# Performance work log

Measured on AMD Instinct MI355X. Metric: run time of the kernel, lower is better.

Reference implementation:

```python
import jax, jax.numpy as jnp
import numpy as np


def _gcn(x, ei, W, b):
    """PyG-style GCNConv: add self-loops, symmetric deg^-1/2 normalization,
    linear transform, scatter-sum aggregation at target nodes, then bias."""
    n = x.shape[0]
    loops = jnp.arange(n)
    src = jnp.concatenate([ei[0], loops])  # message sources
    dst = jnp.concatenate([ei[1], loops])  # aggregation targets
    deg = jax.ops.segment_sum(jnp.ones(src.shape[0], x.dtype), dst, num_segments=n)
    dinv = jnp.where(deg > 0, jax.lax.rsqrt(deg), jnp.zeros_like(deg))
    h = x @ W  # [N, H]
    norm = (dinv[src] * dinv[dst])[:, None]
    out = jax.ops.segment_sum(h[src] * norm, dst, num_segments=n)
    return out + b


def setup_inputs() -> dict:
    N, E, C, H, O, HOPS = 50000, 1600000, 256, 256, 40, 3
    key = jax.random.key(0)
    ks = jax.random.split(key, 12)

    def xav(k, shp):
        # xavier_uniform with relu gain, as in init_weights
        fan_in, fan_out = shp[-2], shp[-1]
        lim = float(np.sqrt(2.0) * np.sqrt(6.0 / (fan_in + fan_out)))
        return jax.random.uniform(k, shp, jnp.float32, -lim, lim)

    return {
        "x": jax.random.normal(ks[0], (N, C), jnp.float32),
        "edge_index": jax.random.randint(ks[1], (2, E), 0, N),
        "new_edge_indexs": jax.random.randint(ks[2], (HOPS, 2, E), 0, N),
        "W_mlp": xav(ks[3], (C, H)),
        "b_mlp": jnp.zeros((H,), jnp.float32),
        "We1": xav(ks[4], (C, H)),
        "be1": jnp.zeros((H,), jnp.float32),
        "We2": xav(ks[5], (H, H)),
        "be2": jnp.zeros((H,), jnp.float32),
        "Wh": xav(ks[6], (HOPS, C, H)),
        "bh": jnp.zeros((HOPS, H), jnp.float32),
        "att": jnp.ones((HOPS + 2,), jnp.float32),
        "Wc": xav(ks[7], (H * (HOPS + 2), O)),
        "bc": jnp.zeros((O,), jnp.float32),
    }


def reference(x, edge_index, new_edge_indexs, W_mlp, b_mlp, We1, be1, We2, be2,
              Wh, bh, att, Wc, bc):
    hops = Wh.shape[0]
    mask = jax.nn.softmax(att)  # softmax over branch attention weights

    mlp = jax.nn.relu(x @ W_mlp + b_mlp) * mask[0]

    e = jax.nn.relu(_gcn(x, edge_index, We1, be1))
    # dropout(p=0.5) is identity in eval mode
    e = jax.nn.relu(_gcn(e, edge_index, We2, be2)) * mask[1]

    # NOTE: original code uses mask[i+1] per hop (hop 0 shares mask[1] with extra_conv)
    outs = [jax.nn.relu(_gcn(x, new_edge_indexs[i], Wh[i], bh[i])) * mask[i + 1]
            for i in range(hops)]

    z = jnp.concatenate(outs + [e, mlp], axis=1)  # [N, H*(hops+2)]
    z = z @ Wc + bc
    return jax.nn.log_softmax(z, axis=-1)
```

## Files before the change

kernel.cpp:

```cpp
#include <hip/hip_runtime.h>
#include <hip/hip_bf16.h>

typedef unsigned short u16;
typedef unsigned int u32;
typedef unsigned char u8;

typedef __bf16 bf16x8 __attribute__((ext_vector_type(8)));
typedef float f32x4 __attribute__((ext_vector_type(4)));

__device__ __forceinline__ u16 f2b(float f) {
    u32 u = __float_as_uint(f);
    u32 r = u + 0x7fffu + ((u >> 16) & 1u);
    return (u16)(r >> 16);
}
__device__ __forceinline__ u8 f2e4m3(float v) {
    return (u8)(__builtin_amdgcn_cvt_pk_fp8_f32(v, v, 0, false) & 0xff);
}
__device__ __forceinline__ void acc16(float* a, uint4 v) {
    u32 w[4] = {v.x, v.y, v.z, v.w};
#pragma unroll
    for (int q = 0; q < 4; ++q) {
        auto p0 = __builtin_amdgcn_cvt_pk_f32_fp8(w[q], false);
        auto p1 = __builtin_amdgcn_cvt_pk_f32_fp8(w[q], true);
        a[q * 4 + 0] += p0[0]; a[q * 4 + 1] += p0[1];
        a[q * 4 + 2] += p1[0]; a[q * 4 + 3] += p1[1];
    }
}

#define SA 72
#define BSHIFT 8
#define BMAX 256
#define BCAP 12288
#define BINCHUNK 4096
#define GEMM_SMEM (128 * SA * 2 * 2)

__global__ __launch_bounds__(256) void prep(
    const int* __restrict__ ei, const int* __restrict__ nei, int E, int B, int SETS,
    int* __restrict__ bcnt, u32* __restrict__ binned, int binB,
    const float* __restrict__ x, u16* __restrict__ x16, int PB, int N,
    const float* __restrict__ W_mlp, const float* __restrict__ We1,
    const float* __restrict__ We2, const float* __restrict__ Wh,
    u16* __restrict__ wt, int HOPS,
    const float* __restrict__ Wc, u16* __restrict__ wct, int O, int NB, int WCB,
    const float* __restrict__ att, float* __restrict__ mask) {
    __shared__ u32 ebuf[BINCHUNK];
    __shared__ int hist[BMAX], resv[BMAX], lbase[BMAX], lcur[BMAX], s[BMAX];
    int b = blockIdx.x, t = threadIdx.x;
    if (b < binB * SETS) {
        int cx = b / SETS, set = b % SETS;
        const int* src = (set == 0) ? ei : (nei + (size_t)(set - 1) * 2 * E);
        const int* dst = src + E;
        hist[t] = 0; lcur[t] = 0;
        __syncthreads();
        int base = cx * BINCHUNK;
        int lim = min(base + BINCHUNK, E);
        for (int i = base + t; i < lim; i += 256)
            atomicAdd(&hist[dst[i] >> BSHIFT], 1);
        __syncthreads();
        int h = hist[t];
        if (t < B && h > 0) resv[t] = atomicAdd(&bcnt[set * BMAX + t], h);
        s[t] = h;
        __syncthreads();
        for (int off = 1; off < 256; off <<= 1) {
            int x2 = s[t];
            int add = (t >= off) ? s[t - off] : 0;
            __syncthreads();
            s[t] = x2 + add;
            __syncthreads();
        }
        lbase[t] = s[t] - h;
        __syncthreads();
        for (int i = base + t; i < lim; i += 256) {
            int d = dst[i];
            int bb = d >> BSHIFT;
            int p = atomicAdd(&lcur[bb], 1);
            ebuf[lbase[bb] + p] = (u32)src[i] | ((u32)d << 16);
        }
        __syncthreads();
        int cnt = lim - base;
        for (int i = t; i < cnt; i += 256) {
            u32 pk = ebuf[i];
            int bb = (int)(pk >> (16 + BSHIFT));
            int gpos = resv[bb] + (i - lbase[bb]);
            if (gpos < BCAP)
                binned[((size_t)set * BMAX + bb) * BCAP + gpos] = pk;
        }
        return;
    }
    b -= binB * SETS;
    if (b < PB) {
        long g = (long)b * 256 + t;
        if (g * 4 < (long)N * 256) {
            float4 v = reinterpret_cast<const float4*>(x)[g];
            ushort4 o; o.x = f2b(v.x); o.y = f2b(v.y); o.z = f2b(v.z); o.w = f2b(v.w);
            reinterpret_cast<ushort4*>(x16)[g] = o;
        }
        return;
    }
    b -= PB;
    int WB = (3 + HOPS) * 256;
    if (b < WB) {
        int y = b >> 8, ib = b & 255;
        const float* W = (y == 0) ? W_mlp : (y == 1) ? We1 : (y == 2) ? We2
                                          : (Wh + (size_t)(y - 3) * 65536);
        int idx = ib * 256 + t;
        int n = idx >> 8, k = idx & 255;
        wt[(size_t)y * 65536 + idx] = f2b(W[k * 256 + n]);
        return;
    }
    b -= WB;
    if (b < WCB) {
        int idx = b * 256 + t;
        if (idx < NB * 48 * 256) {
            int bb = idx / (48 * 256), r = idx - bb * 48 * 256;
            int n = r >> 8, k = r & 255;
            float v = (n < O) ? Wc[((size_t)(bb * 256 + k)) * O + n] : 0.f;
            wct[idx] = f2b(v);
        }
        return;
    }
    if (t == 0) {
        float m = -3.4e38f;
        for (int i = 0; i < NB; ++i) m = fmaxf(m, att[i]);
        float s2 = 0.f;
        for (int i = 0; i < NB; ++i) { float e = __expf(att[i] - m); mask[i] = e; s2 += e; }
        for (int i = 0; i < NB; ++i) mask[i] /= s2;
    }
}

__global__ void bscan(const int* __restrict__ bcnt, int* __restrict__ bbase,
                      int* __restrict__ rp, int N, int E, int B) {
    int set = blockIdx.x, t = threadIdx.x;
    int v = (t < B) ? bcnt[set * BMAX + t] : 0;
    __shared__ int s[256];
    s[t] = v; __syncthreads();
    for (int off = 1; off < 256; off <<= 1) {
        int x = s[t];
        int add = (t >= off) ? s[t - off] : 0;
        __syncthreads();
        s[t] = x + add;
        __syncthreads();
    }
    bbase[set * BMAX + t] = s[t] - v;
    if (t == 0) rp[(size_t)set * (N + 1) + N] = E;
}

__global__ __launch_bounds__(256) void bucket_build(
    const u32* __restrict__ binned, const int* __restrict__ bcnt,
    const int* __restrict__ bbase, int* __restrict__ rp, float* __restrict__ dinv,
    u16* __restrict__ colAll, int E, int N) {
    int set = blockIdx.y;
    int b = blockIdx.x;
    int t = threadIdx.x;
    int nb = bcnt[set * BMAX + b];
    int base = bbase[set * BMAX + b];
    const u32* bin = binned + ((size_t)set * BMAX + b) * BCAP;
    __shared__ int s[256], lcur[256];
    s[t] = 0; lcur[t] = 0;
    __syncthreads();
    for (int i = t; i < nb; i += 256)
        atomicAdd(&s[(bin[i] >> 16) & 255], 1);
    __syncthreads();
    int deg = s[t];
    __syncthreads();
    for (int off = 1; off < 256; off <<= 1) {
        int x = s[t];
        int add = (t >= off) ? s[t - off] : 0;
        __syncthreads();
        s[t] = x + add;
        __syncthreads();
    }
    int ex = s[t] - deg;
    __syncthreads();
    s[t] = ex;
    int node = (b << BSHIFT) + t;
    if (node < N) {
        rp[(size_t)set * (N + 1) + node] = base + ex;
        dinv[(size_t)set * N + node] = rsqrtf((float)(deg + 1));
    }
    __syncthreads();
    for (int i = t; i < nb; i += 256) {
        u32 pk = bin[i];
        int dl = (int)((pk >> 16) & 255);
        int pos = base + s[dl] + atomicAdd(&lcur[dl], 1);
        colAll[(size_t)set * E + pos] = (u16)(pk & 0xffffu);
    }
}

__device__ __forceinline__ void gemm_body(char* smemraw, int bx, int by,
                                          const u16* __restrict__ A, const u16* __restrict__ Bt,
                                          void* __restrict__ outv, const float* bias,
                                          const float* dinv, int mode,
                                          const float* maskp, int M) {
    u16* lsA = (u16*)smemraw;
    u16* lsB = (u16*)(smemraw + 128 * SA * 2);
    const int tid = threadIdx.x;
    const int rowBase = bx * 128, colBase = by * 128;
    const int w = tid >> 6, l = tid & 63;
    const int wm = w >> 1, wn = w & 1;
    const int lrow = l & 15, lkg = l >> 4;
    f32x4 acc[4][4] = {};
    for (int kt = 0; kt < 4; ++kt) {
        const int k0 = kt * 64;
#pragma unroll
        for (int q = 0; q < 4; ++q) {
            int g = q * 256 + tid;
            int m = g >> 3, gq = g & 7;
            int grow = rowBase + m;
            int k = k0 + gq * 8;
            uint4 v = make_uint4(0, 0, 0, 0);
            if (grow < M) v = *reinterpret_cast<const uint4*>(A + (size_t)grow * 256 + k);
            *reinterpret_cast<uint4*>(&lsA[m * SA + gq * 8]) = v;
            uint4 vb = *reinterpret_cast<const uint4*>(Bt + (size_t)(colBase + m) * 256 + k);
            *reinterpret_cast<uint4*>(&lsB[m * SA + gq * 8]) = vb;
        }
        __syncthreads();
#pragma unroll
        for (int kk = 0; kk < 2; ++kk) {
            bf16x8 af[4], bfr[4];
            int kg8 = (kk * 4 + lkg) * 8;
#pragma unroll
            for (int mf = 0; mf < 4; ++mf)
                af[mf] = *reinterpret_cast<const bf16x8*>(&lsA[(wm * 64 + mf * 16 + lrow) * SA + kg8]);
#pragma unroll
            for (int nf = 0; nf < 4; ++nf)
                bfr[nf] = *reinterpret_cast<const bf16x8*>(&lsB[(wn * 64 + nf * 16 + lrow) * SA + kg8]);
#pragma unroll
            for (int mf = 0; mf < 4; ++mf)
#pragma unroll
                for (int nf = 0; nf < 4; ++nf)
                    acc[mf][nf] = __builtin_amdgcn_mfma_f32_16x16x32_bf16(af[mf], bfr[nf], acc[mf][nf], 0, 0, 0);
        }
        __syncthreads();
    }
    float mk = (mode == 0) ? maskp[0] : 1.f;
#pragma unroll
    for (int mf = 0; mf < 4; ++mf) {
#pragma unroll
        for (int r = 0; r < 4; ++r) {
            int row = rowBase + wm * 64 + mf * 16 + lkg * 4 + r;
            if (row >= M) continue;
            float dv = (mode == 1) ? dinv[row] : 0.f;
#pragma unroll
            for (int nf = 0; nf < 4; ++nf) {
                int colG = colBase + wn * 64 + nf * 16 + lrow;
                float v = acc[mf][nf][r];
                if (mode == 0) {
                    v = fmaxf(v + bias[colG], 0.f) * mk;
                    ((u16*)outv)[(size_t)row * 256 + colG] = f2b(v);
                } else {
                    ((u8*)outv)[(size_t)row * 256 + colG] = f2e4m3(v * dv);
                }
            }
        }
    }
}

__global__ __launch_bounds__(256) void gemm5(
    const u16* __restrict__ A, const u16* __restrict__ wt,
    u16* b_out, u8* f_h0, u8* f_h1, u8* f_h2, u8* f_e1,
    const float* __restrict__ b_mlp, const float* __restrict__ dinv,
    const float* __restrict__ maskp, int N, int GB) {
    __shared__ alignas(16) char smem[GEMM_SMEM];
    int bid = blockIdx.x;
    int c = bid & 7;
    int k = bid >> 3;
    int g = c + 8 * (k / 10);
    int m = k % 10;
    if (g >= GB) return;
    int br = m >> 1, half = m & 1;
    const u16* Bt; void* out; const float* dv = nullptr; int mode;
    if (br == 0)      { Bt = wt;              out = b_out; mode = 0; }
    else if (br == 1) { Bt = wt + 3 * 65536;  out = f_h0;  mode = 1; dv = dinv + (size_t)1 * N; }
    else if (br == 2) { Bt = wt + 4 * 65536;  out = f_h1;  mode = 1; dv = dinv + (size_t)2 * N; }
    else if (br == 3) { Bt = wt + 5 * 65536;  out = f_h2;  mode = 1; dv = dinv + (size_t)3 * N; }
    else              { Bt = wt + 1 * 65536;  out = f_e1;  mode = 1; dv = dinv; }
    gemm_body(smem, g, half, A, Bt, out, b_mlp, dv, mode, maskp, N);
}

__global__ __launch_bounds__(256) void gemm_k(const u16* __restrict__ A, const u16* __restrict__ Bt,
                                              u8* __restrict__ out, const float* __restrict__ dinv,
                                              int M) {
    __shared__ alignas(16) char smem[GEMM_SMEM];
    gemm_body(smem, blockIdx.x, blockIdx.y, A, Bt, out, nullptr, dinv, 1, nullptr, M);
}

__device__ __forceinline__ void agg_body(int blk, const u8* __restrict__ hp,
                                         const int* __restrict__ rp, const u16* __restrict__ colv,
                                         const float* __restrict__ dinv, const float* __restrict__ bias,
                                         const float* __restrict__ maskp, int maskIdx,
                                         u16* __restrict__ outb, int N) {
    int node = blk * 4 + (threadIdx.x >> 6);
    if (node >= N) return;
    const int l = threadIdx.x & 63;
    const int slot = l >> 4, li = l & 15;
    const uint4* hv = reinterpret_cast<const uint4*>(hp);
    float a[16] = {0.f, 0.f, 0.f, 0.f, 0.f, 0.f, 0.f, 0.f,
                   0.f, 0.f, 0.f, 0.f, 0.f, 0.f, 0.f, 0.f};
    if (slot == 0) {
        uint4 v = hv[(size_t)node * 16 + li];
        acc16(a, v);
    }
    int beg = rp[node], end = rp[node + 1];
    int j = beg;
    for (; j + 16 <= end; j += 16) {
        int s0 = colv[j + slot];
        int s1 = colv[j + 4 + slot];
        int s2 = colv[j + 8 + slot];
        int s3 = colv[j + 12 + slot];
        uint4 v0 = hv[(size_t)s0 * 16 + li];
        uint4 v1 = hv[(size_t)s1 * 16 + li];
        uint4 v2 = hv[(size_t)s2 * 16 + li];
        uint4 v3 = hv[(size_t)s3 * 16 + li];
        acc16(a, v0); acc16(a, v1); acc16(a, v2); acc16(a, v3);
    }
    for (; j + 4 <= end; j += 4) {
        int s = colv[j + slot];
        acc16(a, hv[(size_t)s * 16 + li]);
    }
    if (j + slot < end) {
        int s = colv[j + slot];
        acc16(a, hv[(size_t)s * 16 + li]);
    }
#pragma unroll
    for (int q = 0; q < 16; ++q) {
        a[q] += __shfl_xor(a[q], 16);
        a[q] += __shfl_xor(a[q], 32);
    }
    if (slot == 0) {
        float dv = dinv[node];
        float mk = (maskIdx >= 0) ? maskp[maskIdx] : 1.f;
        int ch = li * 16;
        u32 o[8];
#pragma unroll
        for (int q = 0; q < 8; ++q) {
            float e0 = fmaxf(fmaf(a[2 * q + 0], dv, bias[ch + 2 * q + 0]), 0.f) * mk;
            float e1 = fmaxf(fmaf(a[2 * q + 1], dv, bias[ch + 2 * q + 1]), 0.f) * mk;
            o[q] = (u32)f2b(e0) | ((u32)f2b(e1) << 16);
        }
        uint4* ob = reinterpret_cast<uint4*>(outb) + (size_t)node * 32 + li * 2;
        ob[0] = make_uint4(o[0], o[1], o[2], o[3]);
        ob[1] = make_uint4(o[4], o[5], o[6], o[7]);
    }
}

__global__ __launch_bounds__(256) void agg_gcn(
    const u8* __restrict__ hp, const int* __restrict__ rp, const u16* __restrict__ colv,
    const float* __restrict__ dinv, const float* __restrict__ bias,
    const float* __restrict__ maskp, int maskIdx, u16* __restrict__ outb, int N) {
    agg_body(blockIdx.x, hp, rp, colv, dinv, bias, maskp, maskIdx, outb, N);
}

__global__ __launch_bounds__(256) void agg3(
    const u8* f0, const u8* f1, const u8* f2,
    const int* __restrict__ rp, const u16* __restrict__ colAll,
    const float* __restrict__ dinv, const float* __restrict__ bh,
    const float* __restrict__ maskp, u16* b0, u16* b1, u16* b2, int N, int E, int AB) {
    int j = blockIdx.x / AB;
    int blk = blockIdx.x - j * AB;
    const u8* hp = (j == 0) ? f0 : (j == 1) ? f1 : f2;
    u16* ob = (j == 0) ? b0 : (j == 1) ? b1 : b2;
    int set = j + 1;
    agg_body(blk, hp, rp + (size_t)set * (N + 1), colAll + (size_t)set * E,
             dinv + (size_t)set * N, bh + (size_t)j * 256, maskp, j + 1, ob, N);
}

template <int MODE>
__global__ __launch_bounds__(256) void logit_gemm(const u16* __restrict__ A,
                                                  const u16* __restrict__ Wct,
                                                  const float* __restrict__ bc,
                                                  float* __restrict__ out, int M) {
    int l = threadIdx.x & 63;
    int rowBase = blockIdx.x * 64 + (threadIdx.x >> 6) * 16;
    if (rowBase >= M) return;
    int lrow = l & 15, lkg = l >> 4;
    int ar = rowBase + lrow; if (ar >= M) ar = M - 1;
    f32x4 acc[3] = {};
#pragma unroll
    for (int kt = 0; kt < 8; ++kt) {
        bf16x8 a = *reinterpret_cast<const bf16x8*>(A + (size_t)ar * 256 + kt * 32 + lkg * 8);
#pragma unroll
        for (int nf = 0; nf < 3; ++nf) {
            bf16x8 b = *reinterpret_cast<const bf16x8*>(Wct + (size_t)(nf * 16 + lrow) * 256 + kt * 32 + lkg * 8);
            acc[nf] = __builtin_amdgcn_mfma_f32_16x16x32_bf16(a, b, acc[nf], 0, 0, 0);
        }
    }
    if (MODE != 2) {
#pragma unroll
        for (int nf = 0; nf < 3; ++nf) {
            int col = nf * 16 + lrow;
            if (col < 40) {
#pragma unroll
                for (int r = 0; r < 4; ++r) {
                    int row = rowBase + lkg * 4 + r;
                    if (row < M) {
                        if (MODE == 1) out[(size_t)row * 40 + col] = acc[nf][r] + bc[col];
                        else           out[(size_t)row * 40 + col] += acc[nf][r];
                    }
                }
            }
        }
    } else {
#pragma unroll
        for (int r = 0; r < 4; ++r) {
            int row = rowBase + lkg * 4 + r;
            float z[3];
#pragma unroll
            for (int nf = 0; nf < 3; ++nf) {
                int col = nf * 16 + lrow;
                z[nf] = -3.4e38f;
                if (col < 40 && row < M) z[nf] = out[(size_t)row * 40 + col] + acc[nf][r];
            }
            float m = fmaxf(fmaxf(z[0], z[1]), z[2]);
#pragma unroll
            for (int off = 1; off < 16; off <<= 1) m = fmaxf(m, __shfl_xor(m, off));
            float s = 0.f;
#pragma unroll
            for (int nf = 0; nf < 3; ++nf) s += (z[nf] > -1e38f) ? __expf(z[nf] - m) : 0.f;
#pragma unroll
            for (int off = 1; off < 16; off <<= 1) s += __shfl_xor(s, off);
            float lg = __logf(s);
#pragma unroll
            for (int nf = 0; nf < 3; ++nf) {
                int col = nf * 16 + lrow;
                if (col < 40 && row < M) out[(size_t)row * 40 + col] = z[nf] - m - lg;
            }
        }
    }
}

__global__ __launch_bounds__(256) void logit3(
    const u16* __restrict__ A0, const u16* __restrict__ A1, const u16* __restrict__ A2,
    const u16* __restrict__ wct, float* __restrict__ out, int M) {
    int l = threadIdx.x & 63;
    int rowBase = blockIdx.x * 64 + (threadIdx.x >> 6) * 16;
    if (rowBase >= M) return;
    int lrow = l & 15, lkg = l >> 4;
    int ar = rowBase + lrow; if (ar >= M) ar = M - 1;
    f32x4 acc[3] = {};
#pragma unroll
    for (int br = 0; br < 3; ++br) {
        const u16* A = (br == 0) ? A0 : (br == 1) ? A1 : A2;
        const u16* Wct = wct + (size_t)br * 48 * 256;
#pragma unroll
        for (int kt = 0; kt < 8; ++kt) {
            bf16x8 a = *reinterpret_cast<const bf16x8*>(A + (size_t)ar * 256 + kt * 32 + lkg * 8);
#pragma unroll
            for (int nf = 0; nf < 3; ++nf) {
                bf16x8 b = *reinterpret_cast<const bf16x8*>(Wct + (size_t)(nf * 16 + lrow) * 256 + kt * 32 + lkg * 8);
                acc[nf] = __builtin_amdgcn_mfma_f32_16x16x32_bf16(a, b, acc[nf], 0, 0, 0);
            }
        }
    }
#pragma unroll
    for (int nf = 0; nf < 3; ++nf) {
        int col = nf * 16 + lrow;
        if (col < 40) {
#pragma unroll
            for (int r = 0; r < 4; ++r) {
                int row = rowBase + lkg * 4 + r;
                if (row < M) out[(size_t)row * 40 + col] += acc[nf][r];
            }
        }
    }
}


extern "C" void kernel_launch(void* const* d_in, const int* in_sizes, int n_in,
                              void* d_out, int out_size, void* d_ws, size_t ws_size,
                              hipStream_t stream) {
    (void)n_in; (void)out_size; (void)ws_size;
    const float* x     = (const float*)d_in[0];
    const int*   ei    = (const int*)d_in[1];
    const int*   nei   = (const int*)d_in[2];
    const float* W_mlp = (const float*)d_in[3];
    const float* b_mlp = (const float*)d_in[4];
    const float* We1   = (const float*)d_in[5];
    const float* be1   = (const float*)d_in[6];
    const float* We2   = (const float*)d_in[7];
    const float* be2   = (const float*)d_in[8];
    const float* Wh    = (const float*)d_in[9];
    const float* bh    = (const float*)d_in[10];
    const float* att   = (const float*)d_in[11];
    const float* Wc    = (const float*)d_in[12];
    const float* bc    = (const float*)d_in[13];
    float* out = (float*)d_out;

    const int N    = in_sizes[0] / 256;
    const int E    = in_sizes[1] / 2;
    const int HOPS = in_sizes[10] / 256;
    const int O    = in_sizes[13];
    const int SETS = HOPS + 1;
    const int NB   = HOPS + 2;
    const int B    = (N + 255) >> 8;

    char* p = (char*)d_ws;
    auto carve = [&](size_t bytes) { char* r = p; p += (bytes + 255) & ~(size_t)255; return r; };
    u16* x16 = (u16*)carve((size_t)N * 256 * 2);
    u16* b0  = (u16*)carve((size_t)N * 256 * 2);
    u16* b1  = (u16*)carve((size_t)N * 256 * 2);
    u16* b2  = (u16*)carve((size_t)N * 256 * 2);
    u8*  f0  = (u8*)carve((size_t)N * 256);
    u8*  f1  = (u8*)carve((size_t)N * 256);
    u8*  f2  = (u8*)carve((size_t)N * 256);
    u8*  f3  = (u8*)carve((size_t)N * 256);
    u8*  f4  = (u8*)carve((size_t)N * 256);
    u16* wt  = (u16*)carve((size_t)(3 + HOPS) * 65536 * 2);
    u16* wct = (u16*)carve((size_t)NB * 48 * 256 * 2);
    float* mask = (float*)carve(256);
    float* dinv = (float*)carve((size_t)SETS * N * 4);
    int* rp    = (int*)carve((size_t)SETS * (N + 1) * 4);
    int* bcnt  = (int*)carve((size_t)SETS * BMAX * 4);
    int* bbase = (int*)carve((size_t)SETS * BMAX * 4);
    u16* colAll = (u16*)carve((size_t)SETS * E * 2);
    u32* binned = (u32*)f0;

    const int PB   = (N * 64 + 255) / 256;
    const int WCB  = (NB * 48 * 256 + 255) / 256;
    const int GB   = (N + 127) / 128;
    const int LB   = (N + 63) / 64;
    const int AB   = (N + 3) / 4;
    const int binB = (E + BINCHUNK - 1) / BINCHUNK;
    auto wct_b = [&](int b) { return wct + (size_t)b * 48 * 256; };

    hipMemsetAsync(bcnt, 0, (size_t)SETS * BMAX * 4, stream);
    {
        int grid = binB * SETS + PB + (3 + HOPS) * 256 + WCB + 1;
        prep<<<grid, 256, 0, stream>>>(ei, nei, E, B, SETS, bcnt, binned, binB,
                                       x, x16, PB, N, W_mlp, We1, We2, Wh, wt, HOPS,
                                       Wc, wct, O, NB, WCB, att, mask);
    }
    bscan<<<SETS, 256, 0, stream>>>(bcnt, bbase, rp, N, E, B);
    {
        dim3 g(B, SETS);
        bucket_build<<<g, 256, 0, stream>>>(binned, bcnt, bbase, rp, dinv, colAll, E, N);
    }
    {
        int GBpad = ((GB + 7) / 8) * 8;
        gemm5<<<10 * GBpad, 256, 0, stream>>>(x16, wt, b0, f0, f1, f2, f3,
                                              b_mlp, dinv, mask, N, GB);
    }
    logit_gemm<1><<<LB, 256, 0, stream>>>(b0, wct_b(NB - 1), bc, out, N);
    agg3<<<3 * AB, 256, 0, stream>>>(f0, f1, f2, rp, colAll, dinv, bh, mask,
                                     b0, b1, b2, N, E, AB);
    logit3<<<LB, 256, 0, stream>>>(b0, b1, b2, wct, out, N);
    agg_gcn<<<AB, 256, 0, stream>>>(f3, rp, colAll, dinv, be1, mask, -1, b1, N);
    gemm_k<<<dim3(GB, 2), 256, 0, stream>>>(b1, wt + 2 * 65536, f4, dinv, N);
    agg_gcn<<<AB, 256, 0, stream>>>(f4, rp, colAll, dinv, be2, mask, 1, b0, N);
    logit_gemm<2><<<LB, 256, 0, stream>>>(b0, wct_b(HOPS), bc, out, N);
}
```

Measured before the change: 634.3 us.

## Merge hop and first-GCN aggregations; fuse second GCN GEMM with partial logits

```diff
diff --git a/kernel.cpp b/kernel.cpp
--- a/kernel.cpp
+++ b/kernel.cpp
@@ -258,7 +258,7 @@
 
 __global__ __launch_bounds__(256) void gemm5(
     const u16* __restrict__ A, const u16* __restrict__ wt,
-    u16* b_out, u8* f_h0, u8* f_h1, u8* f_h2, u8* f_e1,
+    u16* bm, u8* f_h0, u8* f_h1, u8* f_h2, u8* f_e1,
     const float* __restrict__ b_mlp, const float* __restrict__ dinv,
     const float* __restrict__ maskp, int N, int GB) {
     __shared__ alignas(16) char smem[GEMM_SMEM];
@@ -270,19 +270,12 @@
     if (g >= GB) return;
     int br = m >> 1, half = m & 1;
     const u16* Bt; void* out; const float* dv = nullptr; int mode;
-    if (br == 0)      { Bt = wt;              out = b_out; mode = 0; }
-    else if (br == 1) { Bt = wt + 3 * 65536;  out = f_h0;  mode = 1; dv = dinv + (size_t)1 * N; }
-    else if (br == 2) { Bt = wt + 4 * 65536;  out = f_h1;  mode = 1; dv = dinv + (size_t)2 * N; }
-    else if (br == 3) { Bt = wt + 5 * 65536;  out = f_h2;  mode = 1; dv = dinv + (size_t)3 * N; }
-    else              { Bt = wt + 1 * 65536;  out = f_e1;  mode = 1; dv = dinv; }
+    if (br == 0)      { Bt = wt;              out = bm;   mode = 0; }
+    else if (br == 1) { Bt = wt + 3 * 65536;  out = f_h0; mode = 1; dv = dinv + (size_t)1 * N; }
+    else if (br == 2) { Bt = wt + 4 * 65536;  out = f_h1; mode = 1; dv = dinv + (size_t)2 * N; }
+    else if (br == 3) { Bt = wt + 5 * 65536;  out = f_h2; mode = 1; dv = dinv + (size_t)3 * N; }
+    else              { Bt = wt + 1 * 65536;  out = f_e1; mode = 1; dv = dinv; }
     gemm_body(smem, g, half, A, Bt, out, b_mlp, dv, mode, maskp, N);
-}
-
-__global__ __launch_bounds__(256) void gemm_k(const u16* __restrict__ A, const u16* __restrict__ Bt,
-                                              u8* __restrict__ out, const float* __restrict__ dinv,
-                                              int M) {
-    __shared__ alignas(16) char smem[GEMM_SMEM];
-    gemm_body(smem, blockIdx.x, blockIdx.y, A, Bt, out, nullptr, dinv, 1, nullptr, M);
 }
 
 __device__ __forceinline__ void agg_body(int blk, const u8* __restrict__ hp,
@@ -351,25 +344,74 @@
     agg_body(blockIdx.x, hp, rp, colv, dinv, bias, maskp, maskIdx, outb, N);
 }
 
-__global__ __launch_bounds__(256) void agg3(
-    const u8* f0, const u8* f1, const u8* f2,
+__global__ __launch_bounds__(256) void agg4(
+    const u8* f0, const u8* f1, const u8* f2, const u8* f3,
     const int* __restrict__ rp, const u16* __restrict__ colAll,
     const float* __restrict__ dinv, const float* __restrict__ bh,
-    const float* __restrict__ maskp, u16* b0, u16* b1, u16* b2, int N, int E, int AB) {
+    const float* __restrict__ be1, const float* __restrict__ maskp,
+    u16* b0, u16* b1, u16* b2, u16* b3, int N, int E, int AB) {
     int j = blockIdx.x / AB;
     int blk = blockIdx.x - j * AB;
-    const u8* hp = (j == 0) ? f0 : (j == 1) ? f1 : f2;
-    u16* ob = (j == 0) ? b0 : (j == 1) ? b1 : b2;
-    int set = j + 1;
-    agg_body(blk, hp, rp + (size_t)set * (N + 1), colAll + (size_t)set * E,
-             dinv + (size_t)set * N, bh + (size_t)j * 256, maskp, j + 1, ob, N);
-}
-
-template <int MODE>
-__global__ __launch_bounds__(256) void logit_gemm(const u16* __restrict__ A,
-                                                  const u16* __restrict__ Wct,
-                                                  const float* __restrict__ bc,
-                                                  float* __restrict__ out, int M) {
+    if (j < 3) {
+        const u8* hp = (j == 0) ? f0 : (j == 1) ? f1 : f2;
+        u16* ob = (j == 0) ? b0 : (j == 1) ? b1 : b2;
+        int set = j + 1;
+        agg_body(blk, hp, rp + (size_t)set * (N + 1), colAll + (size_t)set * E,
+                 dinv + (size_t)set * N, bh + (size_t)j * 256, maskp, j + 1, ob, N);
+    } else {
+        agg_body(blk, f3, rp, colAll, dinv, be1, maskp, -1, b3, N);
+    }
+}
+
+__global__ __launch_bounds__(256) void combo(
+    const u16* __restrict__ Ae, const u16* __restrict__ Bte, u8* __restrict__ f4,
+    const float* __restrict__ dinv,
+    const u16* __restrict__ b0, const u16* __restrict__ b1, const u16* __restrict__ b2,
+    const u16* __restrict__ bm, const u16* __restrict__ wct, int mlpBlk,
+    const float* __restrict__ bc, float* __restrict__ out, int N, int GB) {
+    __shared__ alignas(16) char smem[GEMM_SMEM];
+    int b = blockIdx.x;
+    if (b < GB * 2) {
+        gemm_body(smem, b >> 1, b & 1, Ae, Bte, f4, nullptr, dinv, 1, nullptr, N);
+        return;
+    }
+    b -= GB * 2;
+    int l = threadIdx.x & 63;
+    int rowBase = b * 64 + (threadIdx.x >> 6) * 16;
+    if (rowBase >= N) return;
+    int lrow = l & 15, lkg = l >> 4;
+    int ar = rowBase + lrow; if (ar >= N) ar = N - 1;
+    f32x4 acc[3] = {};
+#pragma unroll
+    for (int br = 0; br < 4; ++br) {
+        const u16* A = (br == 0) ? b0 : (br == 1) ? b1 : (br == 2) ? b2 : bm;
+        const u16* W = wct + (size_t)((br == 3) ? mlpBlk : br) * 48 * 256;
+#pragma unroll
+        for (int kt = 0; kt < 8; ++kt) {
+            bf16x8 a = *reinterpret_cast<const bf16x8*>(A + (size_t)ar * 256 + kt * 32 + lkg * 8);
+#pragma unroll
+            for (int nf = 0; nf < 3; ++nf) {
+                bf16x8 bw = *reinterpret_cast<const bf16x8*>(W + (size_t)(nf * 16 + lrow) * 256 + kt * 32 + lkg * 8);
+                acc[nf] = __builtin_amdgcn_mfma_f32_16x16x32_bf16(a, bw, acc[nf], 0, 0, 0);
+            }
+        }
+    }
+#pragma unroll
+    for (int nf = 0; nf < 3; ++nf) {
+        int col = nf * 16 + lrow;
+        if (col < 40) {
+#pragma unroll
+            for (int r = 0; r < 4; ++r) {
+                int row = rowBase + lkg * 4 + r;
+                if (row < N) out[(size_t)row * 40 + col] = acc[nf][r] + bc[col];
+            }
+        }
+    }
+}
+
+__global__ __launch_bounds__(256) void logit_fin(const u16* __restrict__ A,
+                                                 const u16* __restrict__ Wct,
+                                                 float* __restrict__ out, int M) {
     int l = threadIdx.x & 63;
     int rowBase = blockIdx.x * 64 + (threadIdx.x >> 6) * 16;
     if (rowBase >= M) return;
@@ -385,82 +427,29 @@
             acc[nf] = __builtin_amdgcn_mfma_f32_16x16x32_bf16(a, b, acc[nf], 0, 0, 0);
         }
     }
-    if (MODE != 2) {
+#pragma unroll
+    for (int r = 0; r < 4; ++r) {
+        int row = rowBase + lkg * 4 + r;
+        float z[3];
 #pragma unroll
         for (int nf = 0; nf < 3; ++nf) {
             int col = nf * 16 + lrow;
-            if (col < 40) {
-#pragma unroll
-                for (int r = 0; r < 4; ++r) {
-                    int row = rowBase + lkg * 4 + r;
-                    if (row < M) {
-                        if (MODE == 1) out[(size_t)row * 40 + col] = acc[nf][r] + bc[col];
-                        else           out[(size_t)row * 40 + col] += acc[nf][r];
-                    }
-                }
-            }
-        }
-    } else {
-#pragma unroll
-        for (int r = 0; r < 4; ++r) {
-            int row = rowBase + lkg * 4 + r;
-            float z[3];
-#pragma unroll
-            for (int nf = 0; nf < 3; ++nf) {
-                int col = nf * 16 + lrow;
-                z[nf] = -3.4e38f;
-                if (col < 40 && row < M) z[nf] = out[(size_t)row * 40 + col] + acc[nf][r];
-            }
-            float m = fmaxf(fmaxf(z[0], z[1]), z[2]);
-#pragma unroll
-            for (int off = 1; off < 16; off <<= 1) m = fmaxf(m, __shfl_xor(m, off));
-            float s = 0.f;
-#pragma unroll
-            for (int nf = 0; nf < 3; ++nf) s += (z[nf] > -1e38f) ? __expf(z[nf] - m) : 0.f;
-#pragma unroll
-            for (int off = 1; off < 16; off <<= 1) s += __shfl_xor(s, off);
-            float lg = __logf(s);
-#pragma unroll
-            for (int nf = 0; nf < 3; ++nf) {
-                int col = nf * 16 + lrow;
-                if (col < 40 && row < M) out[(size_t)row * 40 + col] = z[nf] - m - lg;
-            }
-        }
-    }
-}
-
-__global__ __launch_bounds__(256) void logit3(
-    const u16* __restrict__ A0, const u16* __restrict__ A1, const u16* __restrict__ A2,
-    const u16* __restrict__ wct, float* __restrict__ out, int M) {
-    int l = threadIdx.x & 63;
-    int rowBase = blockIdx.x * 64 + (threadIdx.x >> 6) * 16;
-    if (rowBase >= M) return;
-    int lrow = l & 15, lkg = l >> 4;
-    int ar = rowBase + lrow; if (ar >= M) ar = M - 1;
-    f32x4 acc[3] = {};
-#pragma unroll
-    for (int br = 0; br < 3; ++br) {
-        const u16* A = (br == 0) ? A0 : (br == 1) ? A1 : A2;
-        const u16* Wct = wct + (size_t)br * 48 * 256;
-#pragma unroll
-        for (int kt = 0; kt < 8; ++kt) {
-            bf16x8 a = *reinterpret_cast<const bf16x8*>(A + (size_t)ar * 256 + kt * 32 + lkg * 8);
-#pragma unroll
-            for (int nf = 0; nf < 3; ++nf) {
-                bf16x8 b = *reinterpret_cast<const bf16x8*>(Wct + (size_t)(nf * 16 + lrow) * 256 + kt * 32 + lkg * 8);
-                acc[nf] = __builtin_amdgcn_mfma_f32_16x16x32_bf16(a, b, acc[nf], 0, 0, 0);
-            }
-        }
-    }
-#pragma unroll
-    for (int nf = 0; nf < 3; ++nf) {
-        int col = nf * 16 + lrow;
-        if (col < 40) {
-#pragma unroll
-            for (int r = 0; r < 4; ++r) {
-                int row = rowBase + lkg * 4 + r;
-                if (row < M) out[(size_t)row * 40 + col] += acc[nf][r];
-            }
+            z[nf] = -3.4e38f;
+            if (col < 40 && row < M) z[nf] = out[(size_t)row * 40 + col] + acc[nf][r];
+        }
+        float m = fmaxf(fmaxf(z[0], z[1]), z[2]);
+#pragma unroll
+        for (int off = 1; off < 16; off <<= 1) m = fmaxf(m, __shfl_xor(m, off));
+        float s = 0.f;
+#pragma unroll
+        for (int nf = 0; nf < 3; ++nf) s += (z[nf] > -1e38f) ? __expf(z[nf] - m) : 0.f;
+#pragma unroll
+        for (int off = 1; off < 16; off <<= 1) s += __shfl_xor(s, off);
+        float lg = __logf(s);
+#pragma unroll
+        for (int nf = 0; nf < 3; ++nf) {
+            int col = nf * 16 + lrow;
+            if (col < 40 && row < M) out[(size_t)row * 40 + col] = z[nf] - m - lg;
         }
     }
 }
@@ -497,9 +486,11 @@
     char* p = (char*)d_ws;
     auto carve = [&](size_t bytes) { char* r = p; p += (bytes + 255) & ~(size_t)255; return r; };
     u16* x16 = (u16*)carve((size_t)N * 256 * 2);
+    u16* bm  = (u16*)carve((size_t)N * 256 * 2);
     u16* b0  = (u16*)carve((size_t)N * 256 * 2);
     u16* b1  = (u16*)carve((size_t)N * 256 * 2);
     u16* b2  = (u16*)carve((size_t)N * 256 * 2);
+    u16* b3  = (u16*)carve((size_t)N * 256 * 2);
     u8*  f0  = (u8*)carve((size_t)N * 256);
     u8*  f1  = (u8*)carve((size_t)N * 256);
     u8*  f2  = (u8*)carve((size_t)N * 256);
@@ -521,7 +512,6 @@
     const int LB   = (N + 63) / 64;
     const int AB   = (N + 3) / 4;
     const int binB = (E + BINCHUNK - 1) / BINCHUNK;
-    auto wct_b = [&](int b) { return wct + (size_t)b * 48 * 256; };
 
     hipMemsetAsync(bcnt, 0, (size_t)SETS * BMAX * 4, stream);
     {
@@ -537,15 +527,13 @@
     }
     {
         int GBpad = ((GB + 7) / 8) * 8;
-        gemm5<<<10 * GBpad, 256, 0, stream>>>(x16, wt, b0, f0, f1, f2, f3,
+        gemm5<<<10 * GBpad, 256, 0, stream>>>(x16, wt, bm, f0, f1, f2, f3,
                                               b_mlp, dinv, mask, N, GB);
     }
-    logit_gemm<1><<<LB, 256, 0, stream>>>(b0, wct_b(NB - 1), bc, out, N);
-    agg3<<<3 * AB, 256, 0, stream>>>(f0, f1, f2, rp, colAll, dinv, bh, mask,
-                                     b0, b1, b2, N, E, AB);
-    logit3<<<LB, 256, 0, stream>>>(b0, b1, b2, wct, out, N);
-    agg_gcn<<<AB, 256, 0, stream>>>(f3, rp, colAll, dinv, be1, mask, -1, b1, N);
-    gemm_k<<<dim3(GB, 2), 256, 0, stream>>>(b1, wt + 2 * 65536, f4, dinv, N);
+    agg4<<<4 * AB, 256, 0, stream>>>(f0, f1, f2, f3, rp, colAll, dinv, bh, be1, mask,
+                                     b0, b1, b2, b3, N, E, AB);
+    combo<<<GB * 2 + LB, 256, 0, stream>>>(b3, wt + 2 * 65536, f4, dinv,
+                                           b0, b1, b2, bm, wct, NB - 1, bc, out, N, GB);
     agg_gcn<<<AB, 256, 0, stream>>>(f4, rp, colAll, dinv, be2, mask, 1, b0, N);
-    logit_gemm<2><<<LB, 256, 0, stream>>>(b0, wct_b(HOPS), bc, out, N);
-}
+    logit_fin<<<LB, 256, 0, stream>>>(b0, wct + (size_t)HOPS * 48 * 256, out, N);
+}
```

Result: faster. 609.3 us (-3.9%).
